# Optimization experiments

Hardware: AMD Instinct MI355X
Metric: run time of the kernel (lower is better)

## Reference

```python
import jax, jax.numpy as jnp
import numpy as np


def fwht(x):
    """Unnormalized Fast Walsh-Hadamard transform along axis 0 (Sylvester order).
    Equivalent to H @ x where H is the +/-1 Hadamard matrix. x.shape[0] must be a power of 2."""
    D = x.shape[0]
    orig_shape = x.shape
    x = x.reshape(D, -1)
    h = 1
    while h < D:
        x = x.reshape(D // (2 * h), 2, h, -1)
        a = x[:, 0]
        b = x[:, 1]
        x = jnp.stack([a + b, a - b], axis=1)
        h *= 2
    return x.reshape(orig_shape)


def setup_inputs() -> dict:
    D = 4096
    B = 2048
    key = jax.random.key(0)
    k_x, k_eps, k_rho = jax.random.split(key, 3)
    x = jax.random.normal(k_x, (B, D), dtype=jnp.float32)
    epsilon = jax.random.normal(k_eps, (D,), dtype=jnp.float32)
    s1 = jnp.ones((D,), dtype=jnp.float32) * 0.01
    s2 = jnp.ones((D,), dtype=jnp.float32) * 0.01
    g_mu = jnp.zeros((D,), dtype=jnp.float32)
    # g_rho ~ Uniform(-5, -4) as in the torch init
    g_rho = jax.random.uniform(k_rho, (D,), dtype=jnp.float32, minval=-5.0, maxval=-4.0)
    return {"x": x, "epsilon": epsilon, "s1": s1, "s2": s2, "g_mu": g_mu, "g_rho": g_rho}


def reference(x, epsilon, s1, s2, g_mu, g_rho):
    D = s1.shape[0]
    # g_sigma_sqrt_diagonal = softplus(g_rho); sampled diag g = g_mu + sigma * eps.
    # W = diag(s1) @ H @ diag(g) @ H @ diag(s2); mu and sigma terms are linear in g, so combine.
    g = g_mu + jax.nn.softplus(g_rho) * epsilon
    # HS2 = H * s2 (columns of H scaled by s2) = H @ diag(s2) = fwht(diag(s2)) along axis 0
    HS2 = fwht(jnp.diag(s2))                      # [D, D]
    W = s1[:, None] * fwht(g[:, None] * HS2)      # [D, D]
    # F.linear(x, W) = x @ W^T
    return x @ W.T
```

## Files before the change

kernel.cpp:

```cpp
#include <hip/hip_runtime.h>
#include <math.h>

#define DIM 4096
#define ROWS 2048
#define LSTR 65

__global__ void g_precompute(const float* __restrict__ eps,
                             const float* __restrict__ g_mu,
                             const float* __restrict__ g_rho,
                             float* __restrict__ g_t) {
    int t = blockIdx.x * blockDim.x + threadIdx.x;
    int lp = t >> 6, m = t & 63;
    int j = 256 * (lp >> 2) + 4 * m + (lp & 3);
    float sp = log1pf(expf(g_rho[j]));
    g_t[t] = g_mu[j] + sp * eps[j];
}

__device__ __forceinline__ float4 f4mul(float4 a, float4 b) {
    return make_float4(a.x * b.x, a.y * b.y, a.z * b.z, a.w * b.w);
}

__device__ __forceinline__ void fwht_ri(float4 v[16]) {
#pragma unroll
    for (int j = 0; j < 16; ++j) {
        float4 a = v[j];
        float t0 = a.x + a.y, t1 = a.x - a.y;
        float t2 = a.z + a.w, t3 = a.z - a.w;
        v[j] = make_float4(t0 + t2, t1 + t3, t0 - t2, t1 - t3);
    }
#pragma unroll
    for (int m = 1; m < 16; m <<= 1) {
#pragma unroll
        for (int j = 0; j < 16; ++j) {
            if (!(j & m)) {
                int k = j | m;
                float4 a = v[j], b = v[k];
                v[j] = make_float4(a.x + b.x, a.y + b.y, a.z + b.z, a.w + b.w);
                v[k] = make_float4(a.x - b.x, a.y - b.y, a.z - b.z, a.w - b.w);
            }
        }
    }
}

__device__ __forceinline__ void fwht_m(float f[64]) {
#pragma unroll
    for (int s = 0; s < 6; ++s) {
        const int h = 1 << s;
#pragma unroll
        for (int m = 0; m < 64; ++m) {
            if (!(m & h)) {
                const int k = m | h;
                float a = f[m], b = f[k];
                f[m] = a + b;
                f[k] = a - b;
            }
        }
    }
}

__global__ void __launch_bounds__(256)
whvi_main(const float* __restrict__ x, const float* __restrict__ s1,
          const float* __restrict__ s2, const float* __restrict__ g_t,
          float* __restrict__ out) {
    const int lane = threadIdx.x & 63;
    const int wid  = threadIdx.x >> 6;
    const int row  = blockIdx.x * 4 + wid;

    __shared__ float lds[4 * 64 * LSTR];
    float* __restrict__ L = lds + wid * 64 * LSTR;

    const float4* __restrict__ xr  = (const float4*)(x + (size_t)row * DIM);
    float4* __restrict__       orw = (float4*)(out + (size_t)row * DIM);
    const float4* __restrict__ s2v = (const float4*)s2;
    const float4* __restrict__ s1v = (const float4*)s1;
    const float4* __restrict__ gtv = (const float4*)g_t;

    float4 v[16];
#pragma unroll
    for (int r = 0; r < 16; ++r)
        v[r] = f4mul(xr[64 * r + lane], s2v[64 * r + lane]);

    fwht_ri(v);

#pragma unroll
    for (int r = 0; r < 16; ++r) {
        L[lane * LSTR + 4 * r + 0] = v[r].x;
        L[lane * LSTR + 4 * r + 1] = v[r].y;
        L[lane * LSTR + 4 * r + 2] = v[r].z;
        L[lane * LSTR + 4 * r + 3] = v[r].w;
    }
    float f[64];
#pragma unroll
    for (int m = 0; m < 64; ++m)
        f[m] = L[m * LSTR + lane];

    fwht_m(f);

#pragma unroll
    for (int k = 0; k < 16; ++k) {
        float4 gg = gtv[lane * 16 + k];
        f[4 * k + 0] *= gg.x;
        f[4 * k + 1] *= gg.y;
        f[4 * k + 2] *= gg.z;
        f[4 * k + 3] *= gg.w;
    }

    fwht_m(f);

#pragma unroll
    for (int m = 0; m < 64; ++m)
        L[lane * LSTR + m] = f[m];
#pragma unroll
    for (int r = 0; r < 16; ++r) {
        v[r].x = L[(4 * r + 0) * LSTR + lane];
        v[r].y = L[(4 * r + 1) * LSTR + lane];
        v[r].z = L[(4 * r + 2) * LSTR + lane];
        v[r].w = L[(4 * r + 3) * LSTR + lane];
    }

    fwht_ri(v);

#pragma unroll
    for (int r = 0; r < 16; ++r)
        orw[64 * r + lane] = f4mul(v[r], s1v[64 * r + lane]);
}

extern "C" void kernel_launch(void* const* d_in, const int* in_sizes, int n_in,
                              void* d_out, int out_size, void* d_ws, size_t ws_size,
                              hipStream_t stream) {
    const float* x     = (const float*)d_in[0];
    const float* eps   = (const float*)d_in[1];
    const float* s1    = (const float*)d_in[2];
    const float* s2    = (const float*)d_in[3];
    const float* g_mu  = (const float*)d_in[4];
    const float* g_rho = (const float*)d_in[5];
    float* out = (float*)d_out;
    float* g_t = (float*)d_ws;

    g_precompute<<<DIM / 256, 256, 0, stream>>>(eps, g_mu, g_rho, g_t);
    whvi_main<<<ROWS / 4, 256, 0, stream>>>(x, s1, s2, g_t, out);
}
```

Measured before the change: 100.9 us.

## Fuse softplus gain computation into main kernel and drop precompute launch

Removes the separate g_precompute kernel and computes g = g_mu + softplus(g_rho)*eps inline in every wave, using fast __expf/__logf. This saves one kernel launch and the workspace round trip, but each of the 2048 rows now recomputes 64 exp/log pairs per lane and does three strided scalar gathers instead of one float4 load. It also aliases the float4 and scalar register arrays into one buffer and adds a min-2-blocks launch bound, which can change register allocation.

```diff
diff --git a/kernel.cpp b/kernel.cpp
--- a/kernel.cpp
+++ b/kernel.cpp
@@ -4,17 +4,6 @@
 #define DIM 4096
 #define ROWS 2048
 #define LSTR 65
-
-__global__ void g_precompute(const float* __restrict__ eps,
-                             const float* __restrict__ g_mu,
-                             const float* __restrict__ g_rho,
-                             float* __restrict__ g_t) {
-    int t = blockIdx.x * blockDim.x + threadIdx.x;
-    int lp = t >> 6, m = t & 63;
-    int j = 256 * (lp >> 2) + 4 * m + (lp & 3);
-    float sp = log1pf(expf(g_rho[j]));
-    g_t[t] = g_mu[j] + sp * eps[j];
-}
 
 __device__ __forceinline__ float4 f4mul(float4 a, float4 b) {
     return make_float4(a.x * b.x, a.y * b.y, a.z * b.z, a.w * b.w);
@@ -58,9 +47,10 @@
     }
 }
 
-__global__ void __launch_bounds__(256)
+__global__ void __launch_bounds__(256, 2)
 whvi_main(const float* __restrict__ x, const float* __restrict__ s1,
-          const float* __restrict__ s2, const float* __restrict__ g_t,
+          const float* __restrict__ s2, const float* __restrict__ eps,
+          const float* __restrict__ g_mu, const float* __restrict__ g_rho,
           float* __restrict__ out) {
     const int lane = threadIdx.x & 63;
     const int wid  = threadIdx.x >> 6;
@@ -73,36 +63,34 @@
     float4* __restrict__       orw = (float4*)(out + (size_t)row * DIM);
     const float4* __restrict__ s2v = (const float4*)s2;
     const float4* __restrict__ s1v = (const float4*)s1;
-    const float4* __restrict__ gtv = (const float4*)g_t;
 
-    float4 v[16];
+    float f[64];
+    float4* F = (float4*)f;
+
 #pragma unroll
     for (int r = 0; r < 16; ++r)
-        v[r] = f4mul(xr[64 * r + lane], s2v[64 * r + lane]);
+        F[r] = f4mul(xr[64 * r + lane], s2v[64 * r + lane]);
 
-    fwht_ri(v);
+    fwht_ri(F);
 
 #pragma unroll
-    for (int r = 0; r < 16; ++r) {
-        L[lane * LSTR + 4 * r + 0] = v[r].x;
-        L[lane * LSTR + 4 * r + 1] = v[r].y;
-        L[lane * LSTR + 4 * r + 2] = v[r].z;
-        L[lane * LSTR + 4 * r + 3] = v[r].w;
-    }
-    float f[64];
+    for (int c = 0; c < 64; ++c)
+        L[lane * LSTR + c] = f[c];
 #pragma unroll
     for (int m = 0; m < 64; ++m)
         f[m] = L[m * LSTR + lane];
 
     fwht_m(f);
 
+    {
+        const int base = 256 * (lane >> 2) + (lane & 3);
 #pragma unroll
-    for (int k = 0; k < 16; ++k) {
-        float4 gg = gtv[lane * 16 + k];
-        f[4 * k + 0] *= gg.x;
-        f[4 * k + 1] *= gg.y;
-        f[4 * k + 2] *= gg.z;
-        f[4 * k + 3] *= gg.w;
+        for (int m = 0; m < 64; ++m) {
+            const int j = base + 4 * m;
+            float u  = __expf(g_rho[j]);
+            float sp = __logf(1.0f + u);
+            f[m] *= fmaf(sp, eps[j], g_mu[j]);
+        }
     }
 
     fwht_m(f);
@@ -111,18 +99,14 @@
     for (int m = 0; m < 64; ++m)
         L[lane * LSTR + m] = f[m];
 #pragma unroll
-    for (int r = 0; r < 16; ++r) {
-        v[r].x = L[(4 * r + 0) * LSTR + lane];
-        v[r].y = L[(4 * r + 1) * LSTR + lane];
-        v[r].z = L[(4 * r + 2) * LSTR + lane];
-        v[r].w = L[(4 * r + 3) * LSTR + lane];
-    }
+    for (int c = 0; c < 64; ++c)
+        f[c] = L[c * LSTR + lane];
 
-    fwht_ri(v);
+    fwht_ri(F);
 
 #pragma unroll
     for (int r = 0; r < 16; ++r)
-        orw[64 * r + lane] = f4mul(v[r], s1v[64 * r + lane]);
+        orw[64 * r + lane] = f4mul(F[r], s1v[64 * r + lane]);
 }
 
 extern "C" void kernel_launch(void* const* d_in, const int* in_sizes, int n_in,
@@ -135,8 +119,6 @@
     const float* g_mu  = (const float*)d_in[4];
     const float* g_rho = (const float*)d_in[5];
     float* out = (float*)d_out;
-    float* g_t = (float*)d_ws;
 
-    g_precompute<<<DIM / 256, 256, 0, stream>>>(eps, g_mu, g_rho, g_t);
-    whvi_main<<<ROWS / 4, 256, 0, stream>>>(x, s1, s2, g_t, out);
+    whvi_main<<<ROWS / 4, 256, 0, stream>>>(x, s1, s2, eps, g_mu, g_rho, out);
 }
```

Measured after the change: 106.1 us. +5.1%, slower.
